# Kernel tuning notes

Measured on AMD Instinct MI355X. Metric: run time of the kernel, lower is better.

## Reference

```python
import jax, jax.numpy as jnp
import numpy as np

B, L = 2, 2048
D_MODEL, D_STATE, D_CONV, EXPAND = 1024, 16, 4, 2
D_INNER = EXPAND * D_MODEL
DT_RANK = (D_MODEL + 15) // 16  # 64


def _ln(x, g, b, eps=1e-5):
    mu = jnp.mean(x, -1, keepdims=True)
    var = jnp.var(x, -1, keepdims=True)
    return (x - mu) / jnp.sqrt(var + eps) * g + b


def setup_inputs():
    key = jax.random.key(0)
    ks = jax.random.split(key, 20)
    rn = lambda k, s, sc=0.02: sc * jax.random.normal(k, s, jnp.float32)
    inp = {
        'x': jax.random.normal(ks[0], (B, L, D_MODEL), jnp.float32),
        'in_proj_w': rn(ks[1], (2 * D_INNER, D_MODEL)),
        'conv_w': rn(ks[2], (D_INNER, 1, D_CONV), 0.1),
        'conv_b': rn(ks[3], (D_INNER,), 0.01),
        'x_proj_w': rn(ks[4], (DT_RANK + 2 * D_STATE, D_INNER)),
        'dt_proj_w': rn(ks[5], (D_INNER, DT_RANK), 0.05),
        'dt_proj_b': jnp.full((D_INNER,), jnp.log(jnp.expm1(0.01)), jnp.float32),
        'A_log': jnp.log(jnp.broadcast_to(jnp.arange(1, D_STATE + 1, dtype=jnp.float32), (D_INNER, D_STATE))),
        'Dp': jnp.ones((D_INNER,), jnp.float32),
        'out_proj_w': rn(ks[6], (D_MODEL, D_INNER)),
        'gate_w': rn(ks[7], (D_MODEL, D_MODEL)),
        'gate_b': rn(ks[8], (D_MODEL,), 0.01),
        'fd_w1': rn(ks[9], (D_MODEL, D_MODEL)),
        'fd_b1': rn(ks[10], (D_MODEL,), 0.01),
        'fd_ln_g': jnp.ones((D_MODEL,), jnp.float32),
        'fd_ln_b': jnp.zeros((D_MODEL,), jnp.float32),
        'fd_w2': rn(ks[11], (D_MODEL, D_MODEL)),
        'fd_b2': rn(ks[12], (D_MODEL,), 0.01),
        'norm_g': jnp.ones((D_MODEL,), jnp.float32),
        'norm_b': jnp.zeros((D_MODEL,), jnp.float32),
        'balance_factor': jnp.float32(0.7),
    }
    return inp


def _mamba(x, in_proj_w, conv_w, conv_b, x_proj_w, dt_proj_w, dt_proj_b, A_log, Dp, out_proj_w):
    xz = x @ in_proj_w.T                       # (B,L,2*d_inner)
    xi, z = jnp.split(xz, 2, axis=-1)
    xc = xi.swapaxes(1, 2)                     # (B,d_inner,L)
    xc = jax.lax.conv_general_dilated(
        xc, conv_w, (1,), [(D_CONV - 1, 0)],
        dimension_numbers=('NCH', 'OIH', 'NCH'),
        feature_group_count=D_INNER) + conv_b[None, :, None]
    xc = jax.nn.silu(xc).swapaxes(1, 2)        # (B,L,d_inner)
    x_dbl = xc @ x_proj_w.T                    # (B,L,dt_rank+2*d_state)
    dt, Bm, Cm = jnp.split(x_dbl, [DT_RANK, DT_RANK + D_STATE], axis=-1)
    delta = jax.nn.softplus(dt @ dt_proj_w.T + dt_proj_b)  # (B,L,d_inner)
    A = -jnp.exp(A_log)                        # (d_inner,d_state)

    def step(h, inp):
        d_t, B_t, C_t, u_t = inp               # (B,di),(B,ds),(B,ds),(B,di)
        h = jnp.exp(d_t[:, :, None] * A) * h + (d_t * u_t)[:, :, None] * B_t[:, None, :]
        y = jnp.einsum('bds,bs->bd', h, C_t)
        return h, y

    h0 = jnp.zeros((x.shape[0], D_INNER, D_STATE), x.dtype)
    xs = (delta.swapaxes(0, 1), Bm.swapaxes(0, 1), Cm.swapaxes(0, 1), xc.swapaxes(0, 1))
    _, ys = jax.lax.scan(step, h0, xs)
    y = ys.swapaxes(0, 1) + xc * Dp
    y = y * jax.nn.silu(z)
    return y @ out_proj_w.T


def reference(x, in_proj_w, conv_w, conv_b, x_proj_w, dt_proj_w, dt_proj_b, A_log, Dp, out_proj_w,
              gate_w, gate_b, fd_w1, fd_b1, fd_ln_g, fd_ln_b, fd_w2, fd_b2, norm_g, norm_b, balance_factor):
    detail = jax.nn.relu(_ln(x @ fd_w1.T + fd_b1, fd_ln_g, fd_ln_b)) @ fd_w2.T + fd_b2
    m = _mamba(x, in_proj_w, conv_w, conv_b, x_proj_w, dt_proj_w, dt_proj_b, A_log, Dp, out_proj_w)
    gate = jax.nn.sigmoid(x @ gate_w.T + gate_b)
    f = jax.nn.sigmoid(balance_factor)
    out = x * gate + (m * f + detail * (1 - f)) * (1 - gate)
    return _ln(out, norm_g, norm_b)
```

## Files before the change

kernel.cpp:

```cpp
#include <hip/hip_runtime.h>
#include <hip/hip_bf16.h>
#include <math.h>

#define BB 2
#define LSEQ 2048
#define TTOK (BB * LSEQ)
#define DM 1024
#define DI 2048
#define DSTATE 16
#define DTRANK 64
#define NCHUNK 32
#define CLEN 64

typedef __hip_bfloat16 bf16;
typedef __attribute__((ext_vector_type(4))) float f32x4;
typedef __attribute__((ext_vector_type(8))) __bf16 bf16x8;
typedef __attribute__((ext_vector_type(4))) unsigned short u16x4;

__device__ __forceinline__ float bf2f(bf16 v) { return __bfloat162float(v); }
__device__ __forceinline__ bf16 f2bf(float v) { return __float2bfloat16(v); }

__device__ __forceinline__ float bfbits2f(unsigned short u) {
    return __uint_as_float(((unsigned int)u) << 16);
}
__device__ __forceinline__ unsigned short f2bfbits(float v) {
    bf16 b = f2bf(v);
    return *reinterpret_cast<unsigned short*>(&b);
}

#define LOG2E 1.44269504f

#define N_CANON 14078977

struct Ptrs21 { const void* p[21]; };

__device__ __forceinline__ int probe_f32(const void* alog) {
    float w1 = ((const float*)alog)[1];
    return (fabsf(w1 - 0.6931472f) < 0.2f) ? 1 : 0;
}

__device__ __forceinline__ void gload_lds16(const void* gp, void* lp) {
    __builtin_amdgcn_global_load_lds(
        (const __attribute__((address_space(1))) void*)gp,
        (__attribute__((address_space(3))) void*)lp,
        16, 0, 0);
}

__global__ __launch_bounds__(256) void cvt_all(
    Ptrs21 ptrs, bf16* __restrict__ canon)
{
    int idx = (blockIdx.x * 256 + threadIdx.x) * 4;
    if (idx >= N_CANON) return;
    const int flag = probe_f32(ptrs.p[9]);
    const int starts[22] = {0,4194304,8388608,9437184,10485760,10493952,
                            10496000,10758144,10889216,10891264,10924032,
                            10926080,13023232,13024256,13025280,13026304,
                            13027328,14075904,14076928,14077952,14078976,
                            14078977};
    int seg = 0;
#pragma unroll
    for (int i = 1; i < 21; ++i) if (idx >= starts[i]) seg = i;

    if (idx + 4 <= starts[seg + 1]) {
        int local = idx - starts[seg];
        int src = local;
        bool zero = false;
        if (seg == 6) {
            int r = local >> 11, c = local & 2047;
            if (r >= DTRANK + 2 * DSTATE) zero = true;
            src = r * 2048 + c;
        }
        float v0, v1, v2, v3;
        if (zero) { v0 = v1 = v2 = v3 = 0.f; }
        else if (flag) {
            const float4 t = *reinterpret_cast<const float4*>(
                                 (const float*)ptrs.p[seg] + src);
            v0 = t.x; v1 = t.y; v2 = t.z; v3 = t.w;
        } else {
            const u16x4 t = *reinterpret_cast<const u16x4*>(
                                (const bf16*)ptrs.p[seg] + src);
            v0 = bfbits2f(t[0]); v1 = bfbits2f(t[1]);
            v2 = bfbits2f(t[2]); v3 = bfbits2f(t[3]);
        }
        u16x4 o;
        o[0] = f2bfbits(v0); o[1] = f2bfbits(v1);
        o[2] = f2bfbits(v2); o[3] = f2bfbits(v3);
        *reinterpret_cast<u16x4*>(canon + idx) = o;
    } else {
        for (int j = 0; j < 4 && idx + j < N_CANON; ++j) {
            int e = idx + j;
            int sg = 0;
#pragma unroll
            for (int i = 1; i < 21; ++i) if (e >= starts[i]) sg = i;
            int local = e - starts[sg];
            int src = local;
            bool zero = false;
            if (sg == 6) {
                int r = local >> 11, c = local & 2047;
                if (r >= DTRANK + 2 * DSTATE) zero = true;
                src = r * 2048 + c;
            }
            float v = 0.f;
            if (!zero) {
                if (flag) v = ((const float*)ptrs.p[sg])[src];
                else      v = bf2f(((const bf16*)ptrs.p[sg])[src]);
            }
            canon[e] = f2bf(v);
        }
    }
}

__global__ __launch_bounds__(256) void gemm_bt(
    const bf16* __restrict__ A, const bf16* __restrict__ W,
    bf16* __restrict__ C, bf16* __restrict__ C2, int nsplit,
    const bf16* __restrict__ bias,
    int M, int N, int K, int lda, int ldw, int ldc, int mode)
{
    __shared__ __align__(16) unsigned short As[128 * 64];
    __shared__ __align__(16) unsigned short Bs[128 * 64];

    const int tid  = threadIdx.x;
    const int lane = tid & 63;
    const int wave = tid >> 6;
    const int m0 = blockIdx.x * 128;
    const int n0 = blockIdx.y * 128;
    const int wm = (wave >> 1) * 64;
    const int wn = (wave & 1) * 64;

    f32x4 acc[4][4];
#pragma unroll
    for (int i = 0; i < 4; ++i)
#pragma unroll
        for (int j = 0; j < 4; ++j)
#pragma unroll
            for (int r = 0; r < 4; ++r) acc[i][j][r] = 0.f;

    const int ml = lane & 15;
    const int kq = lane >> 4;

    for (int k0 = 0; k0 < K; k0 += 64) {
#pragma unroll
        for (int i = 0; i < 4; ++i) {
            int c   = wave * 64 + i * 256 + lane;
            int row = c >> 3;
            int j   = (c & 7) ^ (row & 7);
            gload_lds16(A + (size_t)(m0 + row) * lda + k0 + j * 8,
                        &As[(size_t)(wave * 64 + i * 256) * 8]);
            gload_lds16(W + (size_t)(n0 + row) * ldw + k0 + j * 8,
                        &Bs[(size_t)(wave * 64 + i * 256) * 8]);
        }
        __syncthreads();

#pragma unroll
        for (int kb = 0; kb < 2; ++kb) {
            bf16x8 af[4], bfr[4];
#pragma unroll
            for (int i = 0; i < 4; ++i) {
                int ra = wm + i * 16 + ml;
                int rb = wn + i * 16 + ml;
                int g  = kb * 4 + kq;
                af[i]  = *reinterpret_cast<const bf16x8*>(
                             &As[ra * 64 + (g ^ (ra & 7)) * 8]);
                bfr[i] = *reinterpret_cast<const bf16x8*>(
                             &Bs[rb * 64 + (g ^ (rb & 7)) * 8]);
            }
#pragma unroll
            for (int i = 0; i < 4; ++i)
#pragma unroll
                for (int j = 0; j < 4; ++j)
                    acc[i][j] = __builtin_amdgcn_mfma_f32_16x16x32_bf16(af[i], bfr[j], acc[i][j], 0, 0, 0);
        }
        __syncthreads();
    }

    const int cl = lane & 15;
    const int rq = (lane >> 4) * 4;
#pragma unroll
    for (int j = 0; j < 4; ++j) {
        int col = n0 + wn + j * 16 + cl;
        float bv = bias ? bf2f(bias[col]) : 0.f;
        bf16* Cp = C;
        int colw = col;
        bool first = (col < nsplit);
        if (!first) { Cp = C2; colw = col - nsplit; }
#pragma unroll
        for (int i = 0; i < 4; ++i) {
#pragma unroll
            for (int r = 0; r < 4; ++r) {
                int row = m0 + wm + i * 16 + rq + r;
                float v = acc[i][j][r] + bv;
                if (mode == 4 && first) v = 1.f / (1.f + __expf(-v));
                Cp[(size_t)row * ldc + colw] = f2bf(v);
            }
        }
    }
}

__global__ __launch_bounds__(256, 2) void gemm_wide(
    const bf16* __restrict__ A, const bf16* __restrict__ W,
    bf16* __restrict__ O0, bf16* __restrict__ O1,
    bf16* __restrict__ O2, bf16* __restrict__ O3,
    const bf16* __restrict__ bias,
    int M, int N, int K, int lda, int ldw)
{
    __shared__ __align__(16) unsigned short As[128 * 64];
    __shared__ __align__(16) unsigned short Bs[256 * 64];

    const int tid  = threadIdx.x;
    const int lane = tid & 63;
    const int wave = tid >> 6;
    const int m0 = blockIdx.x * 128;
    const int n0 = blockIdx.y * 256;
    const int wm = (wave >> 1) * 64;
    const int wn = (wave & 1) * 128;

    f32x4 acc[4][8];
#pragma unroll
    for (int i = 0; i < 4; ++i)
#pragma unroll
        for (int j = 0; j < 8; ++j)
#pragma unroll
            for (int r = 0; r < 4; ++r) acc[i][j][r] = 0.f;

    const int ml = lane & 15;
    const int kq = lane >> 4;

    for (int k0 = 0; k0 < K; k0 += 64) {
#pragma unroll
        for (int i = 0; i < 4; ++i) {
            int c   = wave * 64 + i * 256 + lane;
            int row = c >> 3;
            int j   = (c & 7) ^ (row & 7);
            gload_lds16(A + (size_t)(m0 + row) * lda + k0 + j * 8,
                        &As[(size_t)(wave * 64 + i * 256) * 8]);
        }
#pragma unroll
        for (int i = 0; i < 8; ++i) {
            int c   = wave * 64 + i * 256 + lane;
            int row = c >> 3;
            int j   = (c & 7) ^ (row & 7);
            gload_lds16(W + (size_t)(n0 + row) * ldw + k0 + j * 8,
                        &Bs[(size_t)(wave * 64 + i * 256) * 8]);
        }
        __syncthreads();

#pragma unroll
        for (int kb = 0; kb < 2; ++kb) {
            bf16x8 af[4], bfr[8];
#pragma unroll
            for (int i = 0; i < 4; ++i) {
                int ra = wm + i * 16 + ml;
                int g  = kb * 4 + kq;
                af[i] = *reinterpret_cast<const bf16x8*>(
                            &As[ra * 64 + (g ^ (ra & 7)) * 8]);
            }
#pragma unroll
            for (int j = 0; j < 8; ++j) {
                int rb = wn + j * 16 + ml;
                int g  = kb * 4 + kq;
                bfr[j] = *reinterpret_cast<const bf16x8*>(
                             &Bs[rb * 64 + (g ^ (rb & 7)) * 8]);
            }
#pragma unroll
            for (int i = 0; i < 4; ++i)
#pragma unroll
                for (int j = 0; j < 8; ++j)
                    acc[i][j] = __builtin_amdgcn_mfma_f32_16x16x32_bf16(af[i], bfr[j], acc[i][j], 0, 0, 0);
        }
        __syncthreads();
    }

    const int cl = lane & 15;
    const int rq = (lane >> 4) * 4;
#pragma unroll
    for (int j = 0; j < 8; ++j) {
        int col = n0 + wn + j * 16 + cl;
        bf16* Cp; int colw; int ldc; float bv = 0.f; bool sig = false;
        if (col < 2048)      { Cp = O0; colw = col;        ldc = 2048; }
        else if (col < 4096) { Cp = O1; colw = col - 2048; ldc = 2048; }
        else {
            bv = bf2f(bias[col - 4096]);
            if (col < 5120)  { Cp = O2; colw = col - 4096; ldc = 1024; sig = true; }
            else             { Cp = O3; colw = col - 5120; ldc = 1024; }
        }
#pragma unroll
        for (int i = 0; i < 4; ++i) {
#pragma unroll
            for (int r = 0; r < 4; ++r) {
                int row = m0 + wm + i * 16 + rq + r;
                float v = acc[i][j][r] + bv;
                if (sig) v = 1.f / (1.f + __expf(-v));
                Cp[(size_t)row * ldc + colw] = f2bf(v);
            }
        }
    }
}

__global__ __launch_bounds__(256) void gemm_k64(
    const bf16* __restrict__ A, const bf16* __restrict__ W,
    bf16* __restrict__ C, const bf16* __restrict__ bias,
    int lda, int ldw, int ldc)
{
    __shared__ __align__(16) unsigned short As[128 * 64];
    __shared__ __align__(16) unsigned short Bs[128 * 64];

    const int tid  = threadIdx.x;
    const int lane = tid & 63;
    const int wave = tid >> 6;
    const int m0 = blockIdx.x * 128;
    const int n0 = blockIdx.y * 128;
    const int wm = (wave >> 1) * 64;
    const int wn = (wave & 1) * 64;

    f32x4 acc[4][4];
#pragma unroll
    for (int i = 0; i < 4; ++i)
#pragma unroll
        for (int j = 0; j < 4; ++j)
#pragma unroll
            for (int r = 0; r < 4; ++r) acc[i][j][r] = 0.f;

    const int ml = lane & 15;
    const int kq = lane >> 4;

#pragma unroll
    for (int i = 0; i < 4; ++i) {
        int c   = wave * 64 + i * 256 + lane;
        int row = c >> 3;
        int j   = (c & 7) ^ (row & 7);
        gload_lds16(A + (size_t)(m0 + row) * lda + j * 8,
                    &As[(size_t)(wave * 64 + i * 256) * 8]);
        gload_lds16(W + (size_t)(n0 + row) * ldw + j * 8,
                    &Bs[(size_t)(wave * 64 + i * 256) * 8]);
    }
    __syncthreads();

#pragma unroll
    for (int kb = 0; kb < 2; ++kb) {
        bf16x8 af[4], bfr[4];
#pragma unroll
        for (int i = 0; i < 4; ++i) {
            int ra = wm + i * 16 + ml;
            int rb = wn + i * 16 + ml;
            int g  = kb * 4 + kq;
            af[i]  = *reinterpret_cast<const bf16x8*>(
                         &As[ra * 64 + (g ^ (ra & 7)) * 8]);
            bfr[i] = *reinterpret_cast<const bf16x8*>(
                         &Bs[rb * 64 + (g ^ (rb & 7)) * 8]);
        }
#pragma unroll
        for (int i = 0; i < 4; ++i)
#pragma unroll
            for (int j = 0; j < 4; ++j)
                acc[i][j] = __builtin_amdgcn_mfma_f32_16x16x32_bf16(af[i], bfr[j], acc[i][j], 0, 0, 0);
    }

    const int cl = lane & 15;
    const int rq = (lane >> 4) * 4;
#pragma unroll
    for (int j = 0; j < 4; ++j) {
        int col = n0 + wn + j * 16 + cl;
        float bv = bf2f(bias[col]);
#pragma unroll
        for (int i = 0; i < 4; ++i) {
#pragma unroll
            for (int r = 0; r < 4; ++r) {
                int row = m0 + wm + i * 16 + rq + r;
                float v = acc[i][j][r] + bv;
                v = (v > 20.f) ? v : log1pf(__expf(v));
                C[(size_t)row * ldc + col] = f2bf(v);
            }
        }
    }
}

__global__ __launch_bounds__(256) void gemm_splitk(
    const bf16* __restrict__ A, const bf16* __restrict__ W,
    float* __restrict__ P0, float* __restrict__ P1,
    int K_slab, int lda, int ldw)
{
    __shared__ __align__(16) unsigned short As[128 * 64];
    __shared__ __align__(16) unsigned short Bs[128 * 64];

    const int tid  = threadIdx.x;
    const int lane = tid & 63;
    const int wave = tid >> 6;
    const int m0 = blockIdx.x * 128;
    const int kb0 = blockIdx.y * K_slab;
    const int wm = (wave >> 1) * 64;
    const int wn = (wave & 1) * 64;

    f32x4 acc[4][4];
#pragma unroll
    for (int i = 0; i < 4; ++i)
#pragma unroll
        for (int j = 0; j < 4; ++j)
#pragma unroll
            for (int r = 0; r < 4; ++r) acc[i][j][r] = 0.f;

    const int ml = lane & 15;
    const int kq = lane >> 4;

    for (int k0 = kb0; k0 < kb0 + K_slab; k0 += 64) {
#pragma unroll
        for (int i = 0; i < 4; ++i) {
            int c   = wave * 64 + i * 256 + lane;
            int row = c >> 3;
            int j   = (c & 7) ^ (row & 7);
            gload_lds16(A + (size_t)(m0 + row) * lda + k0 + j * 8,
                        &As[(size_t)(wave * 64 + i * 256) * 8]);
            gload_lds16(W + (size_t)row * ldw + k0 + j * 8,
                        &Bs[(size_t)(wave * 64 + i * 256) * 8]);
        }
        __syncthreads();

#pragma unroll
        for (int kb = 0; kb < 2; ++kb) {
            bf16x8 af[4], bfr[4];
#pragma unroll
            for (int i = 0; i < 4; ++i) {
                int ra = wm + i * 16 + ml;
                int rb = wn + i * 16 + ml;
                int g  = kb * 4 + kq;
                af[i]  = *reinterpret_cast<const bf16x8*>(
                             &As[ra * 64 + (g ^ (ra & 7)) * 8]);
                bfr[i] = *reinterpret_cast<const bf16x8*>(
                             &Bs[rb * 64 + (g ^ (rb & 7)) * 8]);
            }
#pragma unroll
            for (int i = 0; i < 4; ++i)
#pragma unroll
                for (int j = 0; j < 4; ++j)
                    acc[i][j] = __builtin_amdgcn_mfma_f32_16x16x32_bf16(af[i], bfr[j], acc[i][j], 0, 0, 0);
        }
        __syncthreads();
    }

    float* Ps = ((blockIdx.y < 4) ? P0 : P1)
              + (size_t)(blockIdx.y & 3) * (TTOK * 128);
    const int cl = lane & 15;
    const int rq = (lane >> 4) * 4;
#pragma unroll
    for (int j = 0; j < 4; ++j) {
        int col = wn + j * 16 + cl;
#pragma unroll
        for (int i = 0; i < 4; ++i) {
#pragma unroll
            for (int r = 0; r < 4; ++r) {
                int row = m0 + wm + i * 16 + rq + r;
                Ps[(size_t)row * 128 + col] = acc[i][j][r];
            }
        }
    }
}

__global__ __launch_bounds__(256) void xdbl_reduce(
    const float* __restrict__ P0, const float* __restrict__ P1,
    bf16* __restrict__ xdbl)
{
    int idx = blockIdx.x * 256 + threadIdx.x;
    const int S = TTOK * 128;
    float s = P0[idx] + P0[idx + S] + P0[idx + 2 * S] + P0[idx + 3 * S]
            + P1[idx] + P1[idx + S] + P1[idx + 2 * S] + P1[idx + 3 * S];
    xdbl[idx] = f2bf(s);
}

__global__ __launch_bounds__(256) void gemm_splitk2(
    const bf16* __restrict__ A, const bf16* __restrict__ W,
    bf16* __restrict__ P, int K_slab, int lda, int ldw)
{
    __shared__ __align__(16) unsigned short As[128 * 64];
    __shared__ __align__(16) unsigned short Bs[128 * 64];

    const int tid  = threadIdx.x;
    const int lane = tid & 63;
    const int wave = tid >> 6;
    const int m0 = blockIdx.x * 128;
    const int n0 = blockIdx.y * 128;
    const int kb0 = blockIdx.z * K_slab;
    const int wm = (wave >> 1) * 64;
    const int wn = (wave & 1) * 64;

    f32x4 acc[4][4];
#pragma unroll
    for (int i = 0; i < 4; ++i)
#pragma unroll
        for (int j = 0; j < 4; ++j)
#pragma unroll
            for (int r = 0; r < 4; ++r) acc[i][j][r] = 0.f;

    const int ml = lane & 15;
    const int kq = lane >> 4;

    for (int k0 = kb0; k0 < kb0 + K_slab; k0 += 64) {
#pragma unroll
        for (int i = 0; i < 4; ++i) {
            int c   = wave * 64 + i * 256 + lane;
            int row = c >> 3;
            int j   = (c & 7) ^ (row & 7);
            gload_lds16(A + (size_t)(m0 + row) * lda + k0 + j * 8,
                        &As[(size_t)(wave * 64 + i * 256) * 8]);
            gload_lds16(W + (size_t)(n0 + row) * ldw + k0 + j * 8,
                        &Bs[(size_t)(wave * 64 + i * 256) * 8]);
        }
        __syncthreads();

#pragma unroll
        for (int kb = 0; kb < 2; ++kb) {
            bf16x8 af[4], bfr[4];
#pragma unroll
            for (int i = 0; i < 4; ++i) {
                int ra = wm + i * 16 + ml;
                int rb = wn + i * 16 + ml;
                int g  = kb * 4 + kq;
                af[i]  = *reinterpret_cast<const bf16x8*>(
                             &As[ra * 64 + (g ^ (ra & 7)) * 8]);
                bfr[i] = *reinterpret_cast<const bf16x8*>(
                             &Bs[rb * 64 + (g ^ (rb & 7)) * 8]);
            }
#pragma unroll
            for (int i = 0; i < 4; ++i)
#pragma unroll
                for (int j = 0; j < 4; ++j)
                    acc[i][j] = __builtin_amdgcn_mfma_f32_16x16x32_bf16(af[i], bfr[j], acc[i][j], 0, 0, 0);
        }
        __syncthreads();
    }

    bf16* Ps = P + (size_t)blockIdx.z * (TTOK * DM);
    const int cl = lane & 15;
    const int rq = (lane >> 4) * 4;
#pragma unroll
    for (int j = 0; j < 4; ++j) {
        int col = n0 + wn + j * 16 + cl;
#pragma unroll
        for (int i = 0; i < 4; ++i) {
#pragma unroll
            for (int r = 0; r < 4; ++r) {
                int row = m0 + wm + i * 16 + rq + r;
                Ps[(size_t)row * DM + col] = f2bf(acc[i][j][r]);
            }
        }
    }
}

__global__ __launch_bounds__(256) void conv_silu(
    const bf16* __restrict__ xi, const bf16* __restrict__ convw,
    const bf16* __restrict__ convb, bf16* __restrict__ xc)
{
    int idx = blockIdx.x * 256 + threadIdx.x;
    int cg = idx & 255;
    int t  = idx >> 8;
    int l = t & (LSEQ - 1);
    int b = t >> 11;
    int c0 = cg * 8;

    bf16x8 wv[4];
#pragma unroll
    for (int k = 0; k < 4; ++k)
        wv[k] = *reinterpret_cast<const bf16x8*>(convw + c0 * 4 + k * 8);
    bf16x8 bv = *reinterpret_cast<const bf16x8*>(convb + c0);

    bf16x8 xv[4];
#pragma unroll
    for (int j = 0; j < 4; ++j) {
        int ll = l - 3 + j;
        if (ll >= 0)
            xv[j] = *reinterpret_cast<const bf16x8*>(
                        xi + ((size_t)(b * LSEQ + ll)) * DI + c0);
        else {
#pragma unroll
            for (int s = 0; s < 8; ++s) xv[j][s] = (__bf16)0.f;
        }
    }

    bf16x8 out;
#pragma unroll
    for (int s = 0; s < 8; ++s) {
        float acc = (float)bv[s];
#pragma unroll
        for (int j = 0; j < 4; ++j) {
            int widx = s * 4 + j;
            acc += (float)xv[j][s] * (float)wv[widx >> 3][widx & 7];
        }
        float sv = acc / (1.f + __expf(-acc));
        out[s] = (__bf16)sv;
    }
    *reinterpret_cast<bf16x8*>(xc + (size_t)t * DI + c0) = out;
}

__global__ __launch_bounds__(256) void scan_reduce(
    const bf16* __restrict__ delta, const bf16* __restrict__ xc,
    const bf16* __restrict__ xdbl, const bf16* __restrict__ A_log,
    float* __restrict__ hend, float* __restrict__ decay)
{
    int g = blockIdx.x * 256 + threadIdx.x;
    int d = g & (DI - 1);
    int chunk = (g >> 11) & (NCHUNK - 1);
    int b = g >> 16;

    float A2[16];
#pragma unroll
    for (int s = 0; s < 16; ++s)
        A2[s] = -__expf(bf2f(A_log[d * DSTATE + s])) * LOG2E;

    float h[16];
#pragma unroll
    for (int s = 0; s < 16; ++s) h[s] = 0.f;
    float cumd = 0.f;

    size_t row0 = (size_t)b * LSEQ + (size_t)chunk * CLEN;
    const bf16* pd = delta + row0 * DI + d;
    const bf16* pu = xc    + row0 * DI + d;
    const bf16* pB = xdbl  + row0 * 128 + DTRANK;

    for (int i = 0; i < CLEN; ++i) {
        float dlt = bf2f(pd[(size_t)i * DI]);
        float u   = bf2f(pu[(size_t)i * DI]);
        bf16x8 B0 = *reinterpret_cast<const bf16x8*>(pB + (size_t)i * 128);
        bf16x8 B1 = *reinterpret_cast<const bf16x8*>(pB + (size_t)i * 128 + 8);
        float du = dlt * u;
        cumd += dlt;
#pragma unroll
        for (int s = 0; s < 8; ++s) {
            h[s]     = exp2f(dlt * A2[s])     * h[s]     + du * (float)B0[s];
            h[s + 8] = exp2f(dlt * A2[s + 8]) * h[s + 8] + du * (float)B1[s];
        }
    }
    size_t o = (size_t)g * 16;
#pragma unroll
    for (int s = 0; s < 16; ++s) {
        hend[o + s]  = h[s];
        decay[o + s] = exp2f(A2[s] * cumd);
    }
}

__global__ __launch_bounds__(256) void scan_carry(
    float* hio, const float* __restrict__ decay)
{
    int g = blockIdx.x * 256 + threadIdx.x;
    int sd = g & (DI * DSTATE - 1);
    int b  = g >> 15;
    size_t base = (size_t)b * NCHUNK * DI * DSTATE + sd;
    float carry = 0.f;
    for (int c = 0; c < NCHUNK; ++c) {
        size_t idx = base + (size_t)c * DI * DSTATE;
        float he = hio[idx];
        float dc = decay[idx];
        hio[idx] = carry;
        carry = dc * carry + he;
    }
}

__global__ __launch_bounds__(256) void scan_apply(
    bf16* dy, const bf16* __restrict__ xc, const bf16* __restrict__ xdbl,
    const bf16* __restrict__ z, const bf16* __restrict__ A_log,
    const bf16* __restrict__ Dp, const float* __restrict__ hin)
{
    int g = blockIdx.x * 256 + threadIdx.x;
    int d = g & (DI - 1);
    int chunk = (g >> 11) & (NCHUNK - 1);
    int b = g >> 16;

    float A2[16];
#pragma unroll
    for (int s = 0; s < 16; ++s)
        A2[s] = -__expf(bf2f(A_log[d * DSTATE + s])) * LOG2E;

    float h[16];
    size_t o = (size_t)g * 16;
#pragma unroll
    for (int s = 0; s < 16; ++s) h[s] = hin[o + s];
    float Dd = bf2f(Dp[d]);

    size_t row0 = (size_t)b * LSEQ + (size_t)chunk * CLEN;
    bf16* pd = dy + row0 * DI + d;
    const bf16* pu = xc + row0 * DI + d;
    const bf16* pz = z  + row0 * DI + d;
    const bf16* pB = xdbl + row0 * 128 + DTRANK;

    for (int i = 0; i < CLEN; ++i) {
        float dlt = bf2f(pd[(size_t)i * DI]);
        float u   = bf2f(pu[(size_t)i * DI]);
        float zz  = bf2f(pz[(size_t)i * DI]);
        bf16x8 B0 = *reinterpret_cast<const bf16x8*>(pB + (size_t)i * 128);
        bf16x8 B1 = *reinterpret_cast<const bf16x8*>(pB + (size_t)i * 128 + 8);
        bf16x8 C0 = *reinterpret_cast<const bf16x8*>(pB + (size_t)i * 128 + DSTATE);
        bf16x8 C1 = *reinterpret_cast<const bf16x8*>(pB + (size_t)i * 128 + DSTATE + 8);
        float du = dlt * u;
        float y = 0.f;
#pragma unroll
        for (int s = 0; s < 8; ++s) {
            h[s]     = exp2f(dlt * A2[s])     * h[s]     + du * (float)B0[s];
            h[s + 8] = exp2f(dlt * A2[s + 8]) * h[s + 8] + du * (float)B1[s];
            y += h[s] * (float)C0[s];
            y += h[s + 8] * (float)C1[s];
        }
        y += u * Dd;
        y *= zz / (1.f + __expf(-zz));
        pd[(size_t)i * DI] = f2bf(y);
    }
}

__global__ __launch_bounds__(256) void ln_relu_kernel(
    const bf16* __restrict__ in, const bf16* __restrict__ g,
    const bf16* __restrict__ bta, bf16* __restrict__ out)
{
    int t = blockIdx.x;
    int tid = threadIdx.x;
    int c0 = tid * 4;
    const bf16* row = in + (size_t)t * DM;
    u16x4 tv = *reinterpret_cast<const u16x4*>(row + c0);
    float v[4];
    float sum = 0.f, sq = 0.f;
#pragma unroll
    for (int i = 0; i < 4; ++i) {
        v[i] = bfbits2f(tv[i]);
        sum += v[i];
        sq  += v[i] * v[i];
    }
#pragma unroll
    for (int off = 32; off; off >>= 1) {
        sum += __shfl_down(sum, off, 64);
        sq  += __shfl_down(sq,  off, 64);
    }
    __shared__ float ssum[4], ssq[4];
    int wave = tid >> 6, lane = tid & 63;
    if (lane == 0) { ssum[wave] = sum; ssq[wave] = sq; }
    __syncthreads();
    sum = ssum[0] + ssum[1] + ssum[2] + ssum[3];
    sq  = ssq[0]  + ssq[1]  + ssq[2]  + ssq[3];
    float mu  = sum * (1.f / DM);
    float var = sq * (1.f / DM) - mu * mu;
    float rs  = rsqrtf(var + 1e-5f);
    u16x4 gv = *reinterpret_cast<const u16x4*>(g + c0);
    u16x4 bv = *reinterpret_cast<const u16x4*>(bta + c0);
    u16x4 ov;
#pragma unroll
    for (int i = 0; i < 4; ++i) {
        float o = (v[i] - mu) * rs * bfbits2f(gv[i]) + bfbits2f(bv[i]);
        ov[i] = f2bfbits(fmaxf(o, 0.f));
    }
    *reinterpret_cast<u16x4*>(out + (size_t)t * DM + c0) = ov;
}

__global__ __launch_bounds__(256) void final_kernel(
    const bf16* __restrict__ x, const bf16* __restrict__ gate,
    const bf16* __restrict__ mP0, const bf16* __restrict__ mP1,
    const bf16* __restrict__ detail,
    const bf16* __restrict__ ng, const bf16* __restrict__ nb,
    const bf16* __restrict__ balance, void* __restrict__ out,
    const void* __restrict__ alog)
{
    int t = blockIdx.x;
    int tid = threadIdx.x;
    int c0 = tid * 4;
    size_t base = (size_t)t * DM + c0;
    const int flag = probe_f32(alog);
    float bfv = bf2f(balance[0]);
    float f = 1.f / (1.f + __expf(-bfv));

    u16x4 xv4 = *reinterpret_cast<const u16x4*>(x + base);
    u16x4 gv4 = *reinterpret_cast<const u16x4*>(gate + base);
    u16x4 p04 = *reinterpret_cast<const u16x4*>(mP0 + base);
    u16x4 p14 = *reinterpret_cast<const u16x4*>(mP1 + base);
    u16x4 dt4 = *reinterpret_cast<const u16x4*>(detail + base);

    float v[4];
    float sum = 0.f, sq = 0.f;
#pragma unroll
    for (int i = 0; i < 4; ++i) {
        float xv = bfbits2f(xv4[i]);
        float gv = bfbits2f(gv4[i]);
        float mv = bfbits2f(p04[i]) + bfbits2f(p14[i]);
        float o  = xv * gv + (mv * f + bfbits2f(dt4[i]) * (1.f - f)) * (1.f - gv);
        v[i] = o;
        sum += o;
        sq  += o * o;
    }
#pragma unroll
    for (int off = 32; off; off >>= 1) {
        sum += __shfl_down(sum, off, 64);
        sq  += __shfl_down(sq,  off, 64);
    }
    __shared__ float ssum[4], ssq[4];
    int wave = tid >> 6, lane = tid & 63;
    if (lane == 0) { ssum[wave] = sum; ssq[wave] = sq; }
    __syncthreads();
    sum = ssum[0] + ssum[1] + ssum[2] + ssum[3];
    sq  = ssq[0]  + ssq[1]  + ssq[2]  + ssq[3];
    float mu  = sum * (1.f / DM);
    float var = sq * (1.f / DM) - mu * mu;
    float rs  = rsqrtf(var + 1e-5f);

    u16x4 ngv = *reinterpret_cast<const u16x4*>(ng + c0);
    u16x4 nbv = *reinterpret_cast<const u16x4*>(nb + c0);
    if (flag) {
        float4 ov;
        ov.x = (v[0] - mu) * rs * bfbits2f(ngv[0]) + bfbits2f(nbv[0]);
        ov.y = (v[1] - mu) * rs * bfbits2f(ngv[1]) + bfbits2f(nbv[1]);
        ov.z = (v[2] - mu) * rs * bfbits2f(ngv[2]) + bfbits2f(nbv[2]);
        ov.w = (v[3] - mu) * rs * bfbits2f(ngv[3]) + bfbits2f(nbv[3]);
        *reinterpret_cast<float4*>((float*)out + base) = ov;
    } else {
        u16x4 ov;
#pragma unroll
        for (int i = 0; i < 4; ++i) {
            float o = (v[i] - mu) * rs * bfbits2f(ngv[i]) + bfbits2f(nbv[i]);
            ov[i] = f2bfbits(o);
        }
        *reinterpret_cast<u16x4*>((bf16*)out + base) = ov;
    }
}

#define HEND_B  8388608u
#define XDBL_B  28835840u
#define XI_B    31457280u
#define Z_B     48234496u
#define XC_B    65011712u
#define H2_B    56623104u
#define P1_B    73400320u
#define GATE_FB 39845888u
#define GATE_MB 81788928u
#define H1_MB   90177536u
#define MERGED_NEED 98566144u

extern "C" void kernel_launch(void* const* d_in, const int* in_sizes, int n_in,
                              void* d_out, int out_size, void* d_ws, size_t ws_size,
                              hipStream_t stream) {
    char* ws = (char*)d_ws;
    bf16* canon = (bf16*)ws;
    bf16* cx    = canon;
    bf16* cwBIG = canon + 4194304;
    bf16* cwg   = canon + 8388608;
    bf16* cconvw= canon + 10485760;
    bf16* cconvb= canon + 10493952;
    bf16* cwxp  = canon + 10496000;
    bf16* cdtw  = canon + 10758144;
    bf16* cdtb  = canon + 10889216;
    bf16* cAlog = canon + 10891264;
    bf16* cDp   = canon + 10924032;
    bf16* cwout = canon + 10926080;
    bf16* cgb   = canon + 13023232;
    bf16* clng  = canon + 13025280;
    bf16* clnb  = canon + 13026304;
    bf16* cw2   = canon + 13027328;
    bf16* cb2   = canon + 14075904;
    bf16* cng   = canon + 14076928;
    bf16* cnb   = canon + 14077952;
    bf16* cbal  = canon + 14078976;

    bf16* xdbl  = (bf16*)(ws + XDBL_B);
    bf16* xi    = (bf16*)(ws + XI_B);
    bf16* z     = (bf16*)(ws + Z_B);
    bf16* xc    = (bf16*)(ws + XC_B);
    bf16* delta = xi;
    bf16* dtl   = xi;
    bf16* h2    = (bf16*)(ws + H2_B);
    bf16* opP0  = xc;
    bf16* opP1  = (bf16*)(ws + P1_B);
    float* hend  = (float*)(ws + HEND_B);
    float* part0 = (float*)d_out;
    float* part1 = (float*)(ws + HEND_B);
    float* decay = (float*)d_out;

    const bool merged = (ws_size >= (size_t)MERGED_NEED);
    bf16* gate = merged ? (bf16*)(ws + GATE_MB) : (bf16*)(ws + GATE_FB);
    bf16* h1   = merged ? (bf16*)(ws + H1_MB)   : (bf16*)(ws + Z_B);

    const int NSPLIT_NONE = 1 << 30;
    const void* alog_raw = d_in[7];

    const int srcmap[21] = {0,1,10,12,2,3,4,5,6,7,8,9,11,13,14,15,16,17,18,19,20};
    Ptrs21 ptrs;
    for (int i = 0; i < 21; ++i) ptrs.p[i] = d_in[srcmap[i]];
    cvt_all<<<((N_CANON + 3) / 4 + 255) / 256, 256, 0, stream>>>(ptrs, canon);

    if (merged) {
        gemm_wide<<<dim3(32, 24), 256, 0, stream>>>(cx, cwBIG, xi, z, gate, h1,
                                                    cgb, TTOK, 6144, DM, DM, DM);
    } else {
        gemm_wide<<<dim3(32, 16), 256, 0, stream>>>(cx, cwBIG, xi, z, gate, h1,
                                                    cgb, TTOK, 4096, DM, DM, DM);
    }
    conv_silu<<<(TTOK * 256) / 256, 256, 0, stream>>>(xi, cconvw, cconvb, xc);
    gemm_splitk<<<dim3(32, 8), 256, 0, stream>>>(xc, cwxp, part0, part1,
                                                 256, DI, DI);
    xdbl_reduce<<<(TTOK * 128) / 256, 256, 0, stream>>>(part0, part1, xdbl);
    gemm_k64<<<dim3(32, 16), 256, 0, stream>>>(xdbl, cdtw, delta, cdtb,
                                               128, DTRANK, DI);
    scan_reduce<<<512, 256, 0, stream>>>(delta, xc, xdbl, cAlog, hend, decay);
    scan_carry<<<256, 256, 0, stream>>>(hend, decay);
    scan_apply<<<512, 256, 0, stream>>>(delta, xc, xdbl, z, cAlog, cDp, hend);
    gemm_splitk2<<<dim3(32, 8, 2), 256, 0, stream>>>(delta, cwout, opP0, 1024, DI, DI);
    if (!merged) {
        gemm_bt<<<dim3(32, 16), 256, 0, stream>>>(cx, cwg, gate, h1, DM, cgb,
                                                  TTOK, 2 * DM, DM, DM, DM, DM, 4);
    }
    ln_relu_kernel<<<TTOK, 256, 0, stream>>>(h1, clng, clnb, h2);
    gemm_bt<<<dim3(32, 8), 256, 0, stream>>>(h2, cw2, dtl, dtl, NSPLIT_NONE, cb2,
                                             TTOK, DM, DM, DM, DM, DM, 0);
    final_kernel<<<TTOK, 256, 0, stream>>>(cx, gate, opP0, opP1, dtl, cng, cnb,
                                           cbal, d_out, alog_raw);
}
```

Baseline: 485.0 us.

## Split scan state across half-waves and swizzle wide GEMM block order

The chunked scan kernels now give each channel two lanes, each owning 8 of the 16 state entries. This doubles the thread count to 1024 blocks and halves per-thread register state and serial work. In the apply pass the two halves combine the output with a cross-lane shuffle, and only one half writes. Separately, the wide GEMM remaps block IDs with an XCD-style swizzle (stride by 8) so that blocks sharing tiles land on the same chiplet for L2 reuse. In exchange, the scans load delta, u and z twice, once per half, and the swizzle hardcodes a grid width of 32.

```diff
diff --git a/kernel.cpp b/kernel.cpp
--- a/kernel.cpp
+++ b/kernel.cpp
@@ -209,8 +209,13 @@
     const int tid  = threadIdx.x;
     const int lane = tid & 63;
     const int wave = tid >> 6;
-    const int m0 = blockIdx.x * 128;
-    const int n0 = blockIdx.y * 256;
+    const int lid = blockIdx.y * gridDim.x + blockIdx.x;
+    const int cpx = (gridDim.x * gridDim.y) >> 3;
+    const int swz = (lid & 7) * cpx + (lid >> 3);
+    const int bx  = swz & 31;
+    const int by  = swz >> 5;
+    const int m0 = bx * 128;
+    const int n0 = by * 256;
     const int wm = (wave >> 1) * 64;
     const int wn = (wave & 1) * 128;
 
@@ -595,41 +600,42 @@
     float* __restrict__ hend, float* __restrict__ decay)
 {
     int g = blockIdx.x * 256 + threadIdx.x;
-    int d = g & (DI - 1);
-    int chunk = (g >> 11) & (NCHUNK - 1);
-    int b = g >> 16;
-
-    float A2[16];
-#pragma unroll
-    for (int s = 0; s < 16; ++s)
-        A2[s] = -__expf(bf2f(A_log[d * DSTATE + s])) * LOG2E;
-
-    float h[16];
-#pragma unroll
-    for (int s = 0; s < 16; ++s) h[s] = 0.f;
+    int lane = g & 63;
+    int half = lane >> 5;
+    int dl   = lane & 31;
+    int w    = g >> 6;
+    int d    = (w & 63) * 32 + dl;
+    int chunk= (w >> 6) & (NCHUNK - 1);
+    int b    = w >> 11;
+
+    float A2[8];
+#pragma unroll
+    for (int s = 0; s < 8; ++s)
+        A2[s] = -__expf(bf2f(A_log[d * DSTATE + half * 8 + s])) * LOG2E;
+
+    float h[8];
+#pragma unroll
+    for (int s = 0; s < 8; ++s) h[s] = 0.f;
     float cumd = 0.f;
 
     size_t row0 = (size_t)b * LSEQ + (size_t)chunk * CLEN;
     const bf16* pd = delta + row0 * DI + d;
     const bf16* pu = xc    + row0 * DI + d;
-    const bf16* pB = xdbl  + row0 * 128 + DTRANK;
+    const bf16* pB = xdbl  + row0 * 128 + DTRANK + half * 8;
 
     for (int i = 0; i < CLEN; ++i) {
         float dlt = bf2f(pd[(size_t)i * DI]);
         float u   = bf2f(pu[(size_t)i * DI]);
-        bf16x8 B0 = *reinterpret_cast<const bf16x8*>(pB + (size_t)i * 128);
-        bf16x8 B1 = *reinterpret_cast<const bf16x8*>(pB + (size_t)i * 128 + 8);
+        bf16x8 B = *reinterpret_cast<const bf16x8*>(pB + (size_t)i * 128);
         float du = dlt * u;
         cumd += dlt;
 #pragma unroll
-        for (int s = 0; s < 8; ++s) {
-            h[s]     = exp2f(dlt * A2[s])     * h[s]     + du * (float)B0[s];
-            h[s + 8] = exp2f(dlt * A2[s + 8]) * h[s + 8] + du * (float)B1[s];
-        }
-    }
-    size_t o = (size_t)g * 16;
-#pragma unroll
-    for (int s = 0; s < 16; ++s) {
+        for (int s = 0; s < 8; ++s)
+            h[s] = exp2f(dlt * A2[s]) * h[s] + du * (float)B[s];
+    }
+    size_t o = (((size_t)(b * NCHUNK + chunk) * DI + d) * DSTATE) + half * 8;
+#pragma unroll
+    for (int s = 0; s < 8; ++s) {
         hend[o + s]  = h[s];
         decay[o + s] = exp2f(A2[s] * cumd);
     }
@@ -658,47 +664,48 @@
     const bf16* __restrict__ Dp, const float* __restrict__ hin)
 {
     int g = blockIdx.x * 256 + threadIdx.x;
-    int d = g & (DI - 1);
-    int chunk = (g >> 11) & (NCHUNK - 1);
-    int b = g >> 16;
-
-    float A2[16];
-#pragma unroll
-    for (int s = 0; s < 16; ++s)
-        A2[s] = -__expf(bf2f(A_log[d * DSTATE + s])) * LOG2E;
-
-    float h[16];
-    size_t o = (size_t)g * 16;
-#pragma unroll
-    for (int s = 0; s < 16; ++s) h[s] = hin[o + s];
+    int lane = g & 63;
+    int half = lane >> 5;
+    int dl   = lane & 31;
+    int w    = g >> 6;
+    int d    = (w & 63) * 32 + dl;
+    int chunk= (w >> 6) & (NCHUNK - 1);
+    int b    = w >> 11;
+
+    float A2[8];
+#pragma unroll
+    for (int s = 0; s < 8; ++s)
+        A2[s] = -__expf(bf2f(A_log[d * DSTATE + half * 8 + s])) * LOG2E;
+
+    float h[8];
+    size_t o = (((size_t)(b * NCHUNK + chunk) * DI + d) * DSTATE) + half * 8;
+#pragma unroll
+    for (int s = 0; s < 8; ++s) h[s] = hin[o + s];
     float Dd = bf2f(Dp[d]);
 
     size_t row0 = (size_t)b * LSEQ + (size_t)chunk * CLEN;
     bf16* pd = dy + row0 * DI + d;
     const bf16* pu = xc + row0 * DI + d;
     const bf16* pz = z  + row0 * DI + d;
-    const bf16* pB = xdbl + row0 * 128 + DTRANK;
+    const bf16* pB = xdbl + row0 * 128 + DTRANK + half * 8;
 
     for (int i = 0; i < CLEN; ++i) {
         float dlt = bf2f(pd[(size_t)i * DI]);
         float u   = bf2f(pu[(size_t)i * DI]);
         float zz  = bf2f(pz[(size_t)i * DI]);
-        bf16x8 B0 = *reinterpret_cast<const bf16x8*>(pB + (size_t)i * 128);
-        bf16x8 B1 = *reinterpret_cast<const bf16x8*>(pB + (size_t)i * 128 + 8);
-        bf16x8 C0 = *reinterpret_cast<const bf16x8*>(pB + (size_t)i * 128 + DSTATE);
-        bf16x8 C1 = *reinterpret_cast<const bf16x8*>(pB + (size_t)i * 128 + DSTATE + 8);
+        bf16x8 B = *reinterpret_cast<const bf16x8*>(pB + (size_t)i * 128);
+        bf16x8 C = *reinterpret_cast<const bf16x8*>(pB + (size_t)i * 128 + DSTATE);
         float du = dlt * u;
         float y = 0.f;
 #pragma unroll
         for (int s = 0; s < 8; ++s) {
-            h[s]     = exp2f(dlt * A2[s])     * h[s]     + du * (float)B0[s];
-            h[s + 8] = exp2f(dlt * A2[s + 8]) * h[s + 8] + du * (float)B1[s];
-            y += h[s] * (float)C0[s];
-            y += h[s + 8] * (float)C1[s];
-        }
+            h[s] = exp2f(dlt * A2[s]) * h[s] + du * (float)B[s];
+            y += h[s] * (float)C[s];
+        }
+        y += __shfl_xor(y, 32, 64);
         y += u * Dd;
         y *= zz / (1.f + __expf(-zz));
-        pd[(size_t)i * DI] = f2bf(y);
+        if (half == 0) pd[(size_t)i * DI] = f2bf(y);
     }
 }
 
@@ -889,9 +896,9 @@
     xdbl_reduce<<<(TTOK * 128) / 256, 256, 0, stream>>>(part0, part1, xdbl);
     gemm_k64<<<dim3(32, 16), 256, 0, stream>>>(xdbl, cdtw, delta, cdtb,
                                                128, DTRANK, DI);
-    scan_reduce<<<512, 256, 0, stream>>>(delta, xc, xdbl, cAlog, hend, decay);
+    scan_reduce<<<1024, 256, 0, stream>>>(delta, xc, xdbl, cAlog, hend, decay);
     scan_carry<<<256, 256, 0, stream>>>(hend, decay);
-    scan_apply<<<512, 256, 0, stream>>>(delta, xc, xdbl, z, cAlog, cDp, hend);
+    scan_apply<<<1024, 256, 0, stream>>>(delta, xc, xdbl, z, cAlog, cDp, hend);
     gemm_splitk2<<<dim3(32, 8, 2), 256, 0, stream>>>(delta, cwout, opP0, 1024, DI, DI);
     if (!merged) {
         gemm_bt<<<dim3(32, 16), 256, 0, stream>>>(cx, cwg, gate, h1, DM, cgb,
```

Result: no change. 478.3 us (-1.4%).
